# Kernel optimization log

Measured on AMD Instinct MI355X. Metric: run time of the kernel, lower is better.

## Reference

```python
import jax, jax.numpy as jnp
import numpy as np
import math

B, S, DIM = 2, 2048, 1024
H, D = 16, 64  # num_head, head_dim; H*D == DIM

def setup_inputs() -> dict:
    key = jax.random.key(0)
    ks = jax.random.split(key, 10)
    s = 0.02
    return {
        "X": jax.random.normal(ks[0], (B, S, DIM), dtype=jnp.float32),
        "mask": jnp.ones((B, S), dtype=jnp.float32),
        "Wq": jax.random.normal(ks[1], (DIM, H * D), dtype=jnp.float32) * s,
        "bq": jnp.zeros((H * D,), dtype=jnp.float32),
        "Wk": jax.random.normal(ks[2], (DIM, H * D), dtype=jnp.float32) * s,
        "bk": jnp.zeros((H * D,), dtype=jnp.float32),
        "Wv": jax.random.normal(ks[3], (DIM, H * D), dtype=jnp.float32) * s,
        "bv": jnp.zeros((H * D,), dtype=jnp.float32),
        "Wo": jax.random.normal(ks[4], (H * D, DIM), dtype=jnp.float32) * s,
        "bo": jnp.zeros((DIM,), dtype=jnp.float32),
    }

def _split_heads(x):
    # [B, S, H*D] -> [B, H, S, D]
    b, s, _ = x.shape
    return x.reshape(b, s, H, D).transpose(0, 2, 1, 3)

def reference(X, mask, Wq, bq, Wk, bk, Wv, bv, Wo, bo):
    Q = _split_heads(X @ Wq + bq)
    K = _split_heads(X @ Wk + bk)
    V = _split_heads(X @ Wv + bv)
    # scaled dot-product attention with additive mask penalty
    dot = jnp.einsum('bhqd,bhkd->bhqk', Q, K) / math.sqrt(D)
    dot = dot - 1e6 * (1.0 - mask[:, None, None, :])
    attn = jax.nn.softmax(dot, axis=-1)
    ctx = jnp.einsum('bhqk,bhkd->bhqd', attn, V)
    # combine heads: [B, H, S, D] -> [B, S, H*D]
    ctx = ctx.transpose(0, 2, 1, 3).reshape(B, S, H * D)
    return ctx @ Wo + bo
```

## Files before the change

kernel.cpp:

```cpp
#include <hip/hip_runtime.h>
#include <cstdint>
#include <cstddef>

typedef __attribute__((ext_vector_type(8))) _Float16 f16x8;
typedef __attribute__((ext_vector_type(4))) _Float16 f16x4;
typedef __attribute__((ext_vector_type(4))) float f32x4;

#define MFMA_16x16x32(a, b, c) __builtin_amdgcn_mfma_f32_16x16x32_f16((a), (b), (c), 0, 0, 0)
#define MFMA_16x16x16(a, b, c) __builtin_amdgcn_mfma_f32_16x16x16f16((a), (b), (c), 0, 0, 0)

static constexpr int kB = 2, kS = 2048, kDim = 1024, kH = 16, kD = 64;
static constexpr int kM = kB * kS;
static constexpr float kQScale = 0.125f * 1.44269504088896340736f;
static constexpr float kPenC = 1.44269504088896340736e6f;

__device__ __forceinline__ void wg_barrier_lds() {
  asm volatile("s_waitcnt lgkmcnt(0)" ::: "memory");
  __builtin_amdgcn_s_barrier();
}

__global__ void cvt_f32_to_f16(const float* __restrict__ in, _Float16* __restrict__ out, int n8) {
  int i = blockIdx.x * blockDim.x + threadIdx.x;
  if (i >= n8) return;
  const float4* p = (const float4*)in + (size_t)i * 2;
  float4 a = p[0], b = p[1];
  f16x8 h;
  h[0] = (_Float16)a.x; h[1] = (_Float16)a.y; h[2] = (_Float16)a.z; h[3] = (_Float16)a.w;
  h[4] = (_Float16)b.x; h[5] = (_Float16)b.y; h[6] = (_Float16)b.z; h[7] = (_Float16)b.w;
  ((f16x8*)out)[i] = h;
}

__global__ void transpose_cvt_w(const float* __restrict__ w0, const float* __restrict__ w1,
                                const float* __restrict__ w2, const float* __restrict__ w3,
                                _Float16* __restrict__ o0, _Float16* __restrict__ o1,
                                _Float16* __restrict__ o2, _Float16* __restrict__ o3) {
  const float* w; _Float16* o;
  switch (blockIdx.z) {
    case 0: w = w0; o = o0; break;
    case 1: w = w1; o = o1; break;
    case 2: w = w2; o = o2; break;
    default: w = w3; o = o3; break;
  }
  __shared__ alignas(16) _Float16 tile[64][72];
  const int kt = blockIdx.x * 64;
  const int nt = blockIdx.y * 64;
  const int tr = threadIdx.x >> 4;
  const int tc = threadIdx.x & 15;
#pragma unroll
  for (int rr = 0; rr < 4; ++rr) {
    int r = rr * 16 + tr;
    float4 v = *(const float4*)&w[(size_t)(kt + r) * kDim + nt + tc * 4];
    f16x4 hv;
    hv[0] = (_Float16)v.x; hv[1] = (_Float16)v.y; hv[2] = (_Float16)v.z; hv[3] = (_Float16)v.w;
    *(f16x4*)&tile[r][tc * 4] = hv;
  }
  __syncthreads();
#pragma unroll
  for (int rr = 0; rr < 4; ++rr) {
    int nl = rr * 16 + tr;
    f16x4 hv;
    hv[0] = tile[tc * 4 + 0][nl];
    hv[1] = tile[tc * 4 + 1][nl];
    hv[2] = tile[tc * 4 + 2][nl];
    hv[3] = tile[tc * 4 + 3][nl];
    *(f16x4*)&o[(size_t)(nt + nl) * kDim + kt + tc * 4] = hv;
  }
}

__global__ __launch_bounds__(256, 2) void gemm_qkv(
    const _Float16* __restrict__ A,
    const _Float16* __restrict__ wt0, const _Float16* __restrict__ wt1, const _Float16* __restrict__ wt2,
    const float* __restrict__ bias0, const float* __restrict__ bias1, const float* __restrict__ bias2,
    _Float16* __restrict__ oq, _Float16* __restrict__ ok, _Float16* __restrict__ ov) {
  const _Float16* Bt; const float* bias; _Float16* out;
  switch (blockIdx.z) {
    case 0: Bt = wt0; bias = bias0; out = oq; break;
    case 1: Bt = wt1; bias = bias1; out = ok; break;
    default: Bt = wt2; bias = bias2; out = ov; break;
  }
  __shared__ alignas(16) _Float16 As[2][128 * 72];
  __shared__ alignas(16) _Float16 Bs[2][128 * 72];
  const int tid = threadIdx.x;
  const int lane = tid & 63;
  const int wave = tid >> 6;
  const int wm = wave & 1, wn = wave >> 1;
  const int l15 = lane & 15, quad = lane >> 4;
  const int m0 = blockIdx.x * 128, n0 = blockIdx.y * 128;

  const int srow = tid >> 3;
  const int skc = (tid & 7) * 8;

  f32x4 acc[4][4] = {};
  f16x8 ra[4], rb[4];

#pragma unroll
  for (int i = 0; i < 4; ++i) {
    int row = srow + 32 * i;
    ra[i] = *(const f16x8*)&A[(size_t)(m0 + row) * kDim + skc];
    rb[i] = *(const f16x8*)&Bt[(size_t)(n0 + row) * kDim + skc];
  }
#pragma unroll
  for (int i = 0; i < 4; ++i) {
    int row = srow + 32 * i;
    *(f16x8*)&As[0][row * 72 + skc] = ra[i];
    *(f16x8*)&Bs[0][row * 72 + skc] = rb[i];
  }

  for (int kt = 0; kt < 16; ++kt) {
    const int cur = kt & 1;
    if (kt + 1 < 16) {
      int k0 = (kt + 1) * 64;
#pragma unroll
      for (int i = 0; i < 4; ++i) {
        int row = srow + 32 * i;
        ra[i] = *(const f16x8*)&A[(size_t)(m0 + row) * kDim + k0 + skc];
        rb[i] = *(const f16x8*)&Bt[(size_t)(n0 + row) * kDim + k0 + skc];
      }
    }
    wg_barrier_lds();
#pragma unroll
    for (int kk = 0; kk < 2; ++kk) {
      f16x8 af[4], bf[4];
#pragma unroll
      for (int t = 0; t < 4; ++t) af[t] = *(const f16x8*)&As[cur][(wm * 64 + t * 16 + l15) * 72 + kk * 32 + quad * 8];
#pragma unroll
      for (int t = 0; t < 4; ++t) bf[t] = *(const f16x8*)&Bs[cur][(wn * 64 + t * 16 + l15) * 72 + kk * 32 + quad * 8];
      __builtin_amdgcn_s_setprio(1);
#pragma unroll
      for (int i = 0; i < 4; ++i)
#pragma unroll
        for (int j = 0; j < 4; ++j)
          acc[i][j] = MFMA_16x16x32(af[i], bf[j], acc[i][j]);
      __builtin_amdgcn_s_setprio(0);
    }
    if (kt + 1 < 16) {
#pragma unroll
      for (int i = 0; i < 4; ++i) {
        int row = srow + 32 * i;
        *(f16x8*)&As[cur ^ 1][row * 72 + skc] = ra[i];
        *(f16x8*)&Bs[cur ^ 1][row * 72 + skc] = rb[i];
      }
    }
  }

  const int mbase = m0 + wm * 64 + quad * 4;
  const int nbase = n0 + wn * 64 + l15;
  if (blockIdx.z == 2) {
#pragma unroll
    for (int j = 0; j < 4; ++j) {
      int n = nbase + j * 16;
      float bv = bias[n];
      int h = n >> 6, d = n & 63;
#pragma unroll
      for (int i = 0; i < 4; ++i) {
        int m = mbase + i * 16;
        int b = m >> 11, s = m & (kS - 1);
        f16x4 hv;
#pragma unroll
        for (int r = 0; r < 4; ++r) hv[r] = (_Float16)(acc[i][j][r] + bv);
        *(f16x4*)&out[((size_t)((b * kH + h) * kD + d)) * kS + s] = hv;
      }
    }
  } else {
    const float osc = (blockIdx.z == 0) ? kQScale : 1.0f;
#pragma unroll
    for (int j = 0; j < 4; ++j) {
      int n = nbase + j * 16;
      float bv = bias[n];
      int h = n >> 6, d = n & 63;
#pragma unroll
      for (int i = 0; i < 4; ++i) {
        int mrow = mbase + i * 16;
#pragma unroll
        for (int r = 0; r < 4; ++r) {
          int m = mrow + r;
          int b = m >> 11, s = m & (kS - 1);
          out[(size_t)(((b * kH + h) * kS) + s) * kD + d] = (_Float16)((acc[i][j][r] + bv) * osc);
        }
      }
    }
  }
}

__global__ __launch_bounds__(256, 2) void attn(
    const _Float16* __restrict__ Q, const _Float16* __restrict__ K,
    const _Float16* __restrict__ V, const float* __restrict__ mask,
    _Float16* __restrict__ ctx) {
  const int id = blockIdx.x;
  const int logical = (id & 7) * 64 + (id >> 3);
  const int bh = logical >> 4;
  const int qblk = logical & 15;
  const int b = bh >> 4;
  const int q0 = qblk * 128;
  const int tid = threadIdx.x, lane = tid & 63, wave = tid >> 6;
  const int l15 = lane & 15, quad = lane >> 4;

  __shared__ alignas(16) _Float16 Ks[2][128 * 72];
  __shared__ alignas(16) _Float16 Vs[2][64 * 136];
  __shared__ alignas(16) float pens[kS];

  const _Float16* Qh = Q + (size_t)bh * kS * kD;
  const _Float16* Kh = K + (size_t)bh * kS * kD;
  const _Float16* Vh = V + (size_t)bh * kS * kD;

#pragma unroll
  for (int i = 0; i < 2; ++i) {
    float4 mv4 = *(const float4*)&mask[(size_t)b * kS + tid * 8 + i * 4];
    float4 pv;
    pv.x = (mv4.x - 1.0f) * kPenC;
    pv.y = (mv4.y - 1.0f) * kPenC;
    pv.z = (mv4.z - 1.0f) * kPenC;
    pv.w = (mv4.w - 1.0f) * kPenC;
    *(float4*)&pens[tid * 8 + i * 4] = pv;
  }

  f16x8 qf[2][2];
#pragma unroll
  for (int t = 0; t < 2; ++t) {
    int qrow = q0 + wave * 32 + t * 16 + l15;
#pragma unroll
    for (int kk = 0; kk < 2; ++kk)
      qf[t][kk] = *(const f16x8*)&Qh[(size_t)qrow * kD + kk * 32 + quad * 8];
  }

  f16x4 ones4;
#pragma unroll
  for (int i = 0; i < 4; ++i) ones4[i] = (_Float16)1.0f;

  f32x4 o_acc[2][4] = {};
  f32x4 l_acc[2] = {};

  const int srow = tid >> 3;
  const int skc = (tid & 7) * 8;
  const int vrow = tid >> 4;
  const int vcol = (tid & 15) * 8;

  f16x8 kreg[4], vreg[4];
#pragma unroll
  for (int i = 0; i < 4; ++i)
    kreg[i] = *(const f16x8*)&Kh[(size_t)(srow + 32 * i) * kD + skc];
#pragma unroll
  for (int i = 0; i < 4; ++i)
    vreg[i] = *(const f16x8*)&Vh[(size_t)(vrow + 16 * i) * kS + vcol];
#pragma unroll
  for (int i = 0; i < 4; ++i)
    *(f16x8*)&Ks[0][(srow + 32 * i) * 72 + skc] = kreg[i];
#pragma unroll
  for (int i = 0; i < 4; ++i)
    *(f16x8*)&Vs[0][(vrow + 16 * i) * 136 + vcol] = vreg[i];

  for (int it = 0; it < 16; ++it) {
    const int cur = it & 1;
    const int kb = it * 128;
    if (it + 1 < 16) {
#pragma unroll
      for (int i = 0; i < 4; ++i)
        kreg[i] = *(const f16x8*)&Kh[(size_t)(kb + 128 + srow + 32 * i) * kD + skc];
#pragma unroll
      for (int i = 0; i < 4; ++i)
        vreg[i] = *(const f16x8*)&Vh[(size_t)(vrow + 16 * i) * kS + kb + 128 + vcol];
    }
    wg_barrier_lds();

#pragma unroll
    for (int colt = 0; colt < 8; ++colt) {
      f32x4 pn = *(const f32x4*)&pens[kb + colt * 16 + quad * 4];
      f16x8 kf0 = *(const f16x8*)&Ks[cur][(colt * 16 + l15) * 72 + quad * 8];
      f16x8 kf1 = *(const f16x8*)&Ks[cur][(colt * 16 + l15) * 72 + 32 + quad * 8];
      f32x4 s0 = pn, s1 = pn;
      s0 = MFMA_16x16x32(kf0, qf[0][0], s0);
      s0 = MFMA_16x16x32(kf1, qf[0][1], s0);
      s1 = MFMA_16x16x32(kf0, qf[1][0], s1);
      s1 = MFMA_16x16x32(kf1, qf[1][1], s1);
      f16x4 vf0 = *(const f16x4*)&Vs[cur][(0 * 16 + l15) * 136 + colt * 16 + quad * 4];
      f16x4 vf1 = *(const f16x4*)&Vs[cur][(1 * 16 + l15) * 136 + colt * 16 + quad * 4];
      f16x4 vf2 = *(const f16x4*)&Vs[cur][(2 * 16 + l15) * 136 + colt * 16 + quad * 4];
      f16x4 vf3 = *(const f16x4*)&Vs[cur][(3 * 16 + l15) * 136 + colt * 16 + quad * 4];
      f16x4 pa0, pa1;
#pragma unroll
      for (int r = 0; r < 4; ++r) {
        pa0[r] = (_Float16)__builtin_exp2f(s0[r]);
        pa1[r] = (_Float16)__builtin_exp2f(s1[r]);
      }
      __builtin_amdgcn_s_setprio(1);
      o_acc[0][0] = MFMA_16x16x16(pa0, vf0, o_acc[0][0]);
      o_acc[0][1] = MFMA_16x16x16(pa0, vf1, o_acc[0][1]);
      o_acc[0][2] = MFMA_16x16x16(pa0, vf2, o_acc[0][2]);
      o_acc[0][3] = MFMA_16x16x16(pa0, vf3, o_acc[0][3]);
      o_acc[1][0] = MFMA_16x16x16(pa1, vf0, o_acc[1][0]);
      o_acc[1][1] = MFMA_16x16x16(pa1, vf1, o_acc[1][1]);
      o_acc[1][2] = MFMA_16x16x16(pa1, vf2, o_acc[1][2]);
      o_acc[1][3] = MFMA_16x16x16(pa1, vf3, o_acc[1][3]);
      l_acc[0] = MFMA_16x16x16(pa0, ones4, l_acc[0]);
      l_acc[1] = MFMA_16x16x16(pa1, ones4, l_acc[1]);
      __builtin_amdgcn_s_setprio(0);
    }

    if (it + 1 < 16) {
#pragma unroll
      for (int i = 0; i < 4; ++i)
        *(f16x8*)&Ks[cur ^ 1][(srow + 32 * i) * 72 + skc] = kreg[i];
#pragma unroll
      for (int i = 0; i < 4; ++i)
        *(f16x8*)&Vs[cur ^ 1][(vrow + 16 * i) * 136 + vcol] = vreg[i];
    }
  }

  const int h = bh & 15;
#pragma unroll
  for (int t = 0; t < 2; ++t) {
    f32x4 linv;
#pragma unroll
    for (int r = 0; r < 4; ++r) linv[r] = 1.0f / l_acc[t][r];
    int qbase = q0 + wave * 32 + t * 16 + quad * 4;
#pragma unroll
    for (int c = 0; c < 4; ++c) {
#pragma unroll
      for (int r = 0; r < 4; ++r) {
        ctx[((size_t)(b * kS + qbase + r)) * kDim + h * kD + c * 16 + l15] =
            (_Float16)(o_acc[t][c][r] * linv[r]);
      }
    }
  }
}

__global__ __launch_bounds__(256, 2) void gemm_out(
    const _Float16* __restrict__ A, const _Float16* __restrict__ Bt,
    const float* __restrict__ bias, float* __restrict__ out) {
  __shared__ alignas(16) _Float16 As[2][64 * 72];
  __shared__ alignas(16) _Float16 Bs[2][128 * 72];
  const int tid = threadIdx.x;
  const int lane = tid & 63;
  const int wave = tid >> 6;
  const int wm = wave & 1, wn = wave >> 1;
  const int l15 = lane & 15, quad = lane >> 4;
  const int m0 = blockIdx.x * 64, n0 = blockIdx.y * 128;

  const int srow = tid >> 3;
  const int skc = (tid & 7) * 8;

  f32x4 acc[2][4] = {};
  f16x8 ra[2], rb[4];

#pragma unroll
  for (int i = 0; i < 2; ++i)
    ra[i] = *(const f16x8*)&A[(size_t)(m0 + srow + 32 * i) * kDim + skc];
#pragma unroll
  for (int i = 0; i < 4; ++i)
    rb[i] = *(const f16x8*)&Bt[(size_t)(n0 + srow + 32 * i) * kDim + skc];
#pragma unroll
  for (int i = 0; i < 2; ++i)
    *(f16x8*)&As[0][(srow + 32 * i) * 72 + skc] = ra[i];
#pragma unroll
  for (int i = 0; i < 4; ++i)
    *(f16x8*)&Bs[0][(srow + 32 * i) * 72 + skc] = rb[i];

  for (int kt = 0; kt < 16; ++kt) {
    const int cur = kt & 1;
    if (kt + 1 < 16) {
      int k0 = (kt + 1) * 64;
#pragma unroll
      for (int i = 0; i < 2; ++i)
        ra[i] = *(const f16x8*)&A[(size_t)(m0 + srow + 32 * i) * kDim + k0 + skc];
#pragma unroll
      for (int i = 0; i < 4; ++i)
        rb[i] = *(const f16x8*)&Bt[(size_t)(n0 + srow + 32 * i) * kDim + k0 + skc];
    }
    wg_barrier_lds();
#pragma unroll
    for (int kk = 0; kk < 2; ++kk) {
      f16x8 af[2], bf[4];
#pragma unroll
      for (int t = 0; t < 2; ++t) af[t] = *(const f16x8*)&As[cur][(wm * 32 + t * 16 + l15) * 72 + kk * 32 + quad * 8];
#pragma unroll
      for (int t = 0; t < 4; ++t) bf[t] = *(const f16x8*)&Bs[cur][(wn * 64 + t * 16 + l15) * 72 + kk * 32 + quad * 8];
      __builtin_amdgcn_s_setprio(1);
#pragma unroll
      for (int i = 0; i < 2; ++i)
#pragma unroll
        for (int j = 0; j < 4; ++j)
          acc[i][j] = MFMA_16x16x32(af[i], bf[j], acc[i][j]);
      __builtin_amdgcn_s_setprio(0);
    }
    if (kt + 1 < 16) {
#pragma unroll
      for (int i = 0; i < 2; ++i)
        *(f16x8*)&As[cur ^ 1][(srow + 32 * i) * 72 + skc] = ra[i];
#pragma unroll
      for (int i = 0; i < 4; ++i)
        *(f16x8*)&Bs[cur ^ 1][(srow + 32 * i) * 72 + skc] = rb[i];
    }
  }

  const int mbase = m0 + wm * 32 + quad * 4;
  const int nbase = n0 + wn * 64 + l15;
#pragma unroll
  for (int j = 0; j < 4; ++j) {
    int n = nbase + j * 16;
    float bv = bias[n];
#pragma unroll
    for (int i = 0; i < 2; ++i) {
      int mrow = mbase + i * 16;
#pragma unroll
      for (int r = 0; r < 4; ++r)
        out[(size_t)(mrow + r) * kDim + n] = acc[i][j][r] + bv;
    }
  }
}

extern "C" void kernel_launch(void* const* d_in, const int* in_sizes, int n_in,
                              void* d_out, int out_size, void* d_ws, size_t ws_size,
                              hipStream_t stream) {
  (void)in_sizes; (void)n_in; (void)out_size; (void)ws_size;
  const float* X    = (const float*)d_in[0];
  const float* mask = (const float*)d_in[1];
  const float* Wq   = (const float*)d_in[2];
  const float* bq   = (const float*)d_in[3];
  const float* Wk   = (const float*)d_in[4];
  const float* bk   = (const float*)d_in[5];
  const float* Wv   = (const float*)d_in[6];
  const float* bv   = (const float*)d_in[7];
  const float* Wo   = (const float*)d_in[8];
  const float* bo   = (const float*)d_in[9];
  float* out = (float*)d_out;

  char* ws = (char*)d_ws;
  _Float16* Xh   = (_Float16*)(ws);
  _Float16* Wqt  = (_Float16*)(ws + ((size_t)8  << 20));
  _Float16* Wkt  = (_Float16*)(ws + ((size_t)10 << 20));
  _Float16* Wvt  = (_Float16*)(ws + ((size_t)12 << 20));
  _Float16* Wot  = (_Float16*)(ws + ((size_t)14 << 20));
  _Float16* Qh   = (_Float16*)(ws + ((size_t)16 << 20));
  _Float16* Kh   = (_Float16*)(ws + ((size_t)24 << 20));
  _Float16* Vh   = (_Float16*)(ws + ((size_t)32 << 20));
  _Float16* Ch   = (_Float16*)(ws + ((size_t)40 << 20));

  cvt_f32_to_f16<<<dim3(kM * kDim / 8 / 256), dim3(256), 0, stream>>>(X, Xh, kM * kDim / 8);
  transpose_cvt_w<<<dim3(16, 16, 4), dim3(256), 0, stream>>>(Wq, Wk, Wv, Wo, Wqt, Wkt, Wvt, Wot);
  gemm_qkv<<<dim3(32, 8, 3), dim3(256), 0, stream>>>(Xh, Wqt, Wkt, Wvt, bq, bk, bv, Qh, Kh, Vh);
  attn<<<dim3(512), dim3(256), 0, stream>>>(Qh, Kh, Vh, mask, Ch);
  gemm_out<<<dim3(64, 8), dim3(256), 0, stream>>>(Ch, Wot, bo, out);
}
```

Baseline: 199.6 us.

## Load A fragments directly from global into registers, bypassing LDS in GEMMs

In the QKV and output projection GEMMs, the A operand is now read straight from global memory into MFMA fragment registers instead of being staged through shared memory. A-fragment registers are double-buffered and the k-loop is unrolled by two, while B still goes through LDS double buffering. This removes the LDS stores and reads for A and halves LDS use, which may raise occupancy. In exchange, each wave re-reads A rows that the other waves sharing the same rows also load, using strided 16-byte per-lane accesses that coalesce worse, and register pressure rises.

```diff
diff --git a/kernel.cpp b/kernel.cpp
--- a/kernel.cpp
+++ b/kernel.cpp
@@ -78,7 +78,6 @@
     case 1: Bt = wt1; bias = bias1; out = ok; break;
     default: Bt = wt2; bias = bias2; out = ov; break;
   }
-  __shared__ alignas(16) _Float16 As[2][128 * 72];
   __shared__ alignas(16) _Float16 Bs[2][128 * 72];
   const int tid = threadIdx.x;
   const int lane = tid & 63;
@@ -90,55 +89,84 @@
   const int srow = tid >> 3;
   const int skc = (tid & 7) * 8;
 
+  const _Float16* Abase = A + (size_t)(m0 + wm * 64 + l15) * kDim + quad * 8;
+
   f32x4 acc[4][4] = {};
-  f16x8 ra[4], rb[4];
-
-#pragma unroll
-  for (int i = 0; i < 4; ++i) {
-    int row = srow + 32 * i;
-    ra[i] = *(const f16x8*)&A[(size_t)(m0 + row) * kDim + skc];
-    rb[i] = *(const f16x8*)&Bt[(size_t)(n0 + row) * kDim + skc];
-  }
-#pragma unroll
-  for (int i = 0; i < 4; ++i) {
-    int row = srow + 32 * i;
-    *(f16x8*)&As[0][row * 72 + skc] = ra[i];
-    *(f16x8*)&Bs[0][row * 72 + skc] = rb[i];
-  }
-
-  for (int kt = 0; kt < 16; ++kt) {
-    const int cur = kt & 1;
-    if (kt + 1 < 16) {
+  f16x8 rb[4];
+  f16x8 afA[2][4], afB[2][4];
+
+#pragma unroll
+  for (int i = 0; i < 4; ++i)
+    rb[i] = *(const f16x8*)&Bt[(size_t)(n0 + srow + 32 * i) * kDim + skc];
+#pragma unroll
+  for (int kk = 0; kk < 2; ++kk)
+#pragma unroll
+    for (int t = 0; t < 4; ++t)
+      afA[kk][t] = *(const f16x8*)(Abase + (size_t)t * 16 * kDim + kk * 32);
+#pragma unroll
+  for (int i = 0; i < 4; ++i)
+    *(f16x8*)&Bs[0][(srow + 32 * i) * 72 + skc] = rb[i];
+
+  for (int kt = 0; kt < 16; kt += 2) {
+    {
       int k0 = (kt + 1) * 64;
 #pragma unroll
-      for (int i = 0; i < 4; ++i) {
-        int row = srow + 32 * i;
-        ra[i] = *(const f16x8*)&A[(size_t)(m0 + row) * kDim + k0 + skc];
-        rb[i] = *(const f16x8*)&Bt[(size_t)(n0 + row) * kDim + k0 + skc];
-      }
-    }
-    wg_barrier_lds();
-#pragma unroll
-    for (int kk = 0; kk < 2; ++kk) {
-      f16x8 af[4], bf[4];
-#pragma unroll
-      for (int t = 0; t < 4; ++t) af[t] = *(const f16x8*)&As[cur][(wm * 64 + t * 16 + l15) * 72 + kk * 32 + quad * 8];
-#pragma unroll
-      for (int t = 0; t < 4; ++t) bf[t] = *(const f16x8*)&Bs[cur][(wn * 64 + t * 16 + l15) * 72 + kk * 32 + quad * 8];
-      __builtin_amdgcn_s_setprio(1);
-#pragma unroll
-      for (int i = 0; i < 4; ++i)
-#pragma unroll
-        for (int j = 0; j < 4; ++j)
-          acc[i][j] = MFMA_16x16x32(af[i], bf[j], acc[i][j]);
-      __builtin_amdgcn_s_setprio(0);
-    }
-    if (kt + 1 < 16) {
-#pragma unroll
-      for (int i = 0; i < 4; ++i) {
-        int row = srow + 32 * i;
-        *(f16x8*)&As[cur ^ 1][row * 72 + skc] = ra[i];
-        *(f16x8*)&Bs[cur ^ 1][row * 72 + skc] = rb[i];
+      for (int i = 0; i < 4; ++i)
+        rb[i] = *(const f16x8*)&Bt[(size_t)(n0 + srow + 32 * i) * kDim + k0 + skc];
+#pragma unroll
+      for (int kk = 0; kk < 2; ++kk)
+#pragma unroll
+        for (int t = 0; t < 4; ++t)
+          afB[kk][t] = *(const f16x8*)(Abase + (size_t)t * 16 * kDim + k0 + kk * 32);
+      wg_barrier_lds();
+#pragma unroll
+      for (int kk = 0; kk < 2; ++kk) {
+        f16x8 bf[4];
+#pragma unroll
+        for (int t = 0; t < 4; ++t) bf[t] = *(const f16x8*)&Bs[0][(wn * 64 + t * 16 + l15) * 72 + kk * 32 + quad * 8];
+        __builtin_amdgcn_s_setprio(1);
+#pragma unroll
+        for (int i = 0; i < 4; ++i)
+#pragma unroll
+          for (int j = 0; j < 4; ++j)
+            acc[i][j] = MFMA_16x16x32(afA[kk][i], bf[j], acc[i][j]);
+        __builtin_amdgcn_s_setprio(0);
+      }
+#pragma unroll
+      for (int i = 0; i < 4; ++i)
+        *(f16x8*)&Bs[1][(srow + 32 * i) * 72 + skc] = rb[i];
+    }
+    {
+      int kt1 = kt + 1;
+      if (kt1 + 1 < 16) {
+        int k0 = (kt1 + 1) * 64;
+#pragma unroll
+        for (int i = 0; i < 4; ++i)
+          rb[i] = *(const f16x8*)&Bt[(size_t)(n0 + srow + 32 * i) * kDim + k0 + skc];
+#pragma unroll
+        for (int kk = 0; kk < 2; ++kk)
+#pragma unroll
+          for (int t = 0; t < 4; ++t)
+            afA[kk][t] = *(const f16x8*)(Abase + (size_t)t * 16 * kDim + k0 + kk * 32);
+      }
+      wg_barrier_lds();
+#pragma unroll
+      for (int kk = 0; kk < 2; ++kk) {
+        f16x8 bf[4];
+#pragma unroll
+        for (int t = 0; t < 4; ++t) bf[t] = *(const f16x8*)&Bs[1][(wn * 64 + t * 16 + l15) * 72 + kk * 32 + quad * 8];
+        __builtin_amdgcn_s_setprio(1);
+#pragma unroll
+        for (int i = 0; i < 4; ++i)
+#pragma unroll
+          for (int j = 0; j < 4; ++j)
+            acc[i][j] = MFMA_16x16x32(afB[kk][i], bf[j], acc[i][j]);
+        __builtin_amdgcn_s_setprio(0);
+      }
+      if (kt1 + 1 < 16) {
+#pragma unroll
+        for (int i = 0; i < 4; ++i)
+          *(f16x8*)&Bs[0][(srow + 32 * i) * 72 + skc] = rb[i];
       }
     }
   }
@@ -327,7 +355,6 @@
 __global__ __launch_bounds__(256, 2) void gemm_out(
     const _Float16* __restrict__ A, const _Float16* __restrict__ Bt,
     const float* __restrict__ bias, float* __restrict__ out) {
-  __shared__ alignas(16) _Float16 As[2][64 * 72];
   __shared__ alignas(16) _Float16 Bs[2][128 * 72];
   const int tid = threadIdx.x;
   const int lane = tid & 63;
@@ -339,56 +366,85 @@
   const int srow = tid >> 3;
   const int skc = (tid & 7) * 8;
 
+  const _Float16* Abase = A + (size_t)(m0 + wm * 32 + l15) * kDim + quad * 8;
+
   f32x4 acc[2][4] = {};
-  f16x8 ra[2], rb[4];
-
-#pragma unroll
-  for (int i = 0; i < 2; ++i)
-    ra[i] = *(const f16x8*)&A[(size_t)(m0 + srow + 32 * i) * kDim + skc];
+  f16x8 rb[4];
+  f16x8 afA[2][2], afB[2][2];
+
 #pragma unroll
   for (int i = 0; i < 4; ++i)
     rb[i] = *(const f16x8*)&Bt[(size_t)(n0 + srow + 32 * i) * kDim + skc];
 #pragma unroll
-  for (int i = 0; i < 2; ++i)
-    *(f16x8*)&As[0][(srow + 32 * i) * 72 + skc] = ra[i];
+  for (int kk = 0; kk < 2; ++kk)
+#pragma unroll
+    for (int t = 0; t < 2; ++t)
+      afA[kk][t] = *(const f16x8*)(Abase + (size_t)t * 16 * kDim + kk * 32);
 #pragma unroll
   for (int i = 0; i < 4; ++i)
     *(f16x8*)&Bs[0][(srow + 32 * i) * 72 + skc] = rb[i];
 
-  for (int kt = 0; kt < 16; ++kt) {
-    const int cur = kt & 1;
-    if (kt + 1 < 16) {
+  for (int kt = 0; kt < 16; kt += 2) {
+    {
       int k0 = (kt + 1) * 64;
 #pragma unroll
-      for (int i = 0; i < 2; ++i)
-        ra[i] = *(const f16x8*)&A[(size_t)(m0 + srow + 32 * i) * kDim + k0 + skc];
-#pragma unroll
       for (int i = 0; i < 4; ++i)
         rb[i] = *(const f16x8*)&Bt[(size_t)(n0 + srow + 32 * i) * kDim + k0 + skc];
-    }
-    wg_barrier_lds();
-#pragma unroll
-    for (int kk = 0; kk < 2; ++kk) {
-      f16x8 af[2], bf[4];
-#pragma unroll
-      for (int t = 0; t < 2; ++t) af[t] = *(const f16x8*)&As[cur][(wm * 32 + t * 16 + l15) * 72 + kk * 32 + quad * 8];
-#pragma unroll
-      for (int t = 0; t < 4; ++t) bf[t] = *(const f16x8*)&Bs[cur][(wn * 64 + t * 16 + l15) * 72 + kk * 32 + quad * 8];
-      __builtin_amdgcn_s_setprio(1);
-#pragma unroll
-      for (int i = 0; i < 2; ++i)
-#pragma unroll
-        for (int j = 0; j < 4; ++j)
-          acc[i][j] = MFMA_16x16x32(af[i], bf[j], acc[i][j]);
-      __builtin_amdgcn_s_setprio(0);
-    }
-    if (kt + 1 < 16) {
-#pragma unroll
-      for (int i = 0; i < 2; ++i)
-        *(f16x8*)&As[cur ^ 1][(srow + 32 * i) * 72 + skc] = ra[i];
-#pragma unroll
-      for (int i = 0; i < 4; ++i)
-        *(f16x8*)&Bs[cur ^ 1][(srow + 32 * i) * 72 + skc] = rb[i];
+#pragma unroll
+      for (int kk = 0; kk < 2; ++kk)
+#pragma unroll
+        for (int t = 0; t < 2; ++t)
+          afB[kk][t] = *(const f16x8*)(Abase + (size_t)t * 16 * kDim + k0 + kk * 32);
+      wg_barrier_lds();
+#pragma unroll
+      for (int kk = 0; kk < 2; ++kk) {
+        f16x8 bf[4];
+#pragma unroll
+        for (int t = 0; t < 4; ++t) bf[t] = *(const f16x8*)&Bs[0][(wn * 64 + t * 16 + l15) * 72 + kk * 32 + quad * 8];
+        __builtin_amdgcn_s_setprio(1);
+#pragma unroll
+        for (int i = 0; i < 2; ++i)
+#pragma unroll
+          for (int j = 0; j < 4; ++j)
+            acc[i][j] = MFMA_16x16x32(afA[kk][i], bf[j], acc[i][j]);
+        __builtin_amdgcn_s_setprio(0);
+      }
+#pragma unroll
+      for (int i = 0; i < 4; ++i)
+        *(f16x8*)&Bs[1][(srow + 32 * i) * 72 + skc] = rb[i];
+    }
+    {
+      int kt1 = kt + 1;
+      if (kt1 + 1 < 16) {
+        int k0 = (kt1 + 1) * 64;
+#pragma unroll
+        for (int i = 0; i < 4; ++i)
+          rb[i] = *(const f16x8*)&Bt[(size_t)(n0 + srow + 32 * i) * kDim + k0 + skc];
+#pragma unroll
+        for (int kk = 0; kk < 2; ++kk)
+#pragma unroll
+          for (int t = 0; t < 2; ++t)
+            afA[kk][t] = *(const f16x8*)(Abase + (size_t)t * 16 * kDim + k0 + kk * 32);
+      }
+      wg_barrier_lds();
+#pragma unroll
+      for (int kk = 0; kk < 2; ++kk) {
+        f16x8 bf[4];
+#pragma unroll
+        for (int t = 0; t < 4; ++t) bf[t] = *(const f16x8*)&Bs[1][(wn * 64 + t * 16 + l15) * 72 + kk * 32 + quad * 8];
+        __builtin_amdgcn_s_setprio(1);
+#pragma unroll
+        for (int i = 0; i < 2; ++i)
+#pragma unroll
+          for (int j = 0; j < 4; ++j)
+            acc[i][j] = MFMA_16x16x32(afB[kk][i], bf[j], acc[i][j]);
+        __builtin_amdgcn_s_setprio(0);
+      }
+      if (kt1 + 1 < 16) {
+#pragma unroll
+        for (int i = 0; i < 4; ++i)
+          *(f16x8*)&Bs[0][(srow + 32 * i) * 72 + skc] = rb[i];
+      }
     }
   }
 
```

Result: slower. 224.8 us (+12.6%).
